# Performance work log

Measured on AMD Instinct MI355X. Metric: run time of the kernel, lower is better.

The kernel has to match this reference:

```python
import jax, jax.numpy as jnp
import numpy as np

# Dims
B, S, D = 2, 2048, 1024
H, KV = 16, 4            # rosa heads / kv heads -> n_rep = 4
QKB, VB = 16, 32          # query-key bits / value bits
N_REP = H // KV
TAU = 1.0


def setup_inputs() -> dict:
    key = jax.random.key(0)
    ks = jax.random.split(key, 8)
    sc = lambda fan_in: 1.0 / np.sqrt(fan_in)
    return {
        "hidden_states": jax.random.normal(ks[0], (B, S, D), jnp.float32),
        # Linear weights stored (in, out) so y = x @ W
        "Wq": jax.random.normal(ks[1], (D, H * QKB), jnp.float32) * sc(D),
        "Wk": jax.random.normal(ks[2], (D, KV * QKB), jnp.float32) * sc(D),
        "Wv": jax.random.normal(ks[3], (D, KV * VB), jnp.float32) * sc(D),
        "Wo": jax.random.normal(ks[4], (H * VB, D), jnp.float32) * sc(H * VB),
        "v_emb0": jnp.full((H * VB,), -1e-05, jnp.float32),
        "v_emb1": jnp.full((H * VB,), +1e-05, jnp.float32),
    }


def _repeat_kv(x, n_rep):
    # x: [B, KV, S, d] -> [B, KV*n_rep, S, d]
    b, kv, s, d = x.shape
    return jnp.broadcast_to(x[:, :, None], (b, kv, n_rep, s, d)).reshape(b, kv * n_rep, s, d)


def reference(hidden_states, Wq, Wk, Wv, Wo, v_emb0, v_emb1):
    b, s, _ = hidden_states.shape
    q = (hidden_states @ Wq).reshape(b, s, H, QKB).transpose(0, 2, 1, 3)   # [B,H,S,QKB]
    k = (hidden_states @ Wk).reshape(b, s, KV, QKB).transpose(0, 2, 1, 3)
    v = (hidden_states @ Wv).reshape(b, s, KV, VB).transpose(0, 2, 1, 3)
    k = _repeat_kv(k, N_REP)                                               # [B,H,S,QKB]
    v = _repeat_kv(v, N_REP)                                               # [B,H,S,VB]

    # Soft binarization (hard path uses (x > 0); soft path relaxes with sigmoid(x/tau)).
    pq = jax.nn.sigmoid(q / TAU)
    pk = jax.nn.sigmoid(k / TAU)
    pv = jax.nn.sigmoid(v / TAU)

    # Expected number of matching bits between soft-binary q_i and k_j:
    # sum_b [ pq*pk + (1-pq)(1-pk) ] = QKB - sum(pq) - sum(pk) + 2 * pq.pk
    dot = jnp.einsum("bhsd,bhtd->bhst", pq, pk)                            # [B,H,S,S]
    scores = QKB - pq.sum(-1)[:, :, :, None] - pk.sum(-1)[:, :, None, :] + 2.0 * dot

    causal = jnp.tril(jnp.ones((s, s), bool))                              # [S,S]
    scores = jnp.where(causal[None, None], scores, jnp.finfo(scores.dtype).min)
    attn = jax.nn.softmax(scores / TAU, axis=-1)

    vh = jnp.einsum("bhst,bhtd->bhsd", attn, pv)                           # [B,H,S,VB]
    e0 = v_emb0.reshape(1, H, 1, VB)
    e1 = v_emb1.reshape(1, H, 1, VB)
    out = e0 * (1.0 - vh) + e1 * vh                                        # [B,H,S,VB]
    out = out.transpose(0, 2, 1, 3).reshape(b, s, H * VB)
    return out @ Wo                                                        # [B,S,D]
```

## Files before the change

### kernel.cpp

```cpp
#include <hip/hip_runtime.h>
#include <hip/hip_bf16.h>

#define B_    2
#define S_    2048
#define D_    1024
#define H_    16
#define KV_   4
#define QKB_  16
#define VB_   32
#define NTOK  (B_ * S_)
#define L2E_  1.44269504088896f

typedef __attribute__((ext_vector_type(8))) short bshort8;
typedef __attribute__((ext_vector_type(4))) float f32x4;

__device__ __forceinline__ unsigned short bf16_rne(float x) {
    unsigned u = __float_as_uint(x);
    return (unsigned short)((u + 0x7FFFu + ((u >> 16) & 1u)) >> 16);
}
__device__ __forceinline__ unsigned bf16x2_rne(float lo, float hi) {
    return (unsigned)bf16_rne(lo) | ((unsigned)bf16_rne(hi) << 16);
}
__device__ __forceinline__ unsigned cvt_pk_bf16(float lo, float hi) {
    unsigned r;
    asm("v_cvt_pk_bf16_f32 %0, %1, %2" : "=v"(r) : "v"(lo), "v"(hi));
    return r;
}
__device__ __forceinline__ float sum2bf(unsigned u) {
    return __uint_as_float(u << 16) + __uint_as_float(u & 0xFFFF0000u);
}
__device__ __forceinline__ void stage16(const unsigned short* g, unsigned short* l) {
    __builtin_amdgcn_global_load_lds(
        (const __attribute__((address_space(1))) void*)g,
        (__attribute__((address_space(3))) void*)l, 16, 0, 0);
}

__global__ __launch_bounds__(256) void prep_kernel(
    const float* __restrict__ hs,
    const float* __restrict__ Wq, const float* __restrict__ Wk,
    const float* __restrict__ Wv, const float* __restrict__ Wo,
    unsigned short* __restrict__ hs_b,
    unsigned short* __restrict__ Wcat_t, unsigned short* __restrict__ Wot)
{
    __shared__ float T[64][65];
    const int t = threadIdx.x;
    if (blockIdx.x < 2048) {
        int i = blockIdx.x * 256 + t;
        const float4* s = (const float4*)hs;
        float4 a = s[2 * i], b = s[2 * i + 1];
        uint4 o;
        o.x = bf16x2_rne(a.x, a.y); o.y = bf16x2_rne(a.z, a.w);
        o.z = bf16x2_rne(b.x, b.y); o.w = bf16x2_rne(b.z, b.w);
        ((uint4*)hs_b)[i] = o;
        return;
    }
    const int bid = blockIdx.x - 2048;
    const float* src; unsigned short* dst; int K, N, tk, tn, drow0;
    if (bid < 64)       { src = Wq; dst = Wcat_t; K = 1024; N = 256;  int r = bid;       tk = r & 15; tn = r >> 4; drow0 = 0; }
    else if (bid < 80)  { src = Wk; dst = Wcat_t; K = 1024; N = 64;   int r = bid - 64;  tk = r;      tn = 0;      drow0 = 256; }
    else if (bid < 112) { src = Wv; dst = Wcat_t; K = 1024; N = 128;  int r = bid - 80;  tk = r & 15; tn = r >> 4; drow0 = 320; }
    else                { src = Wo; dst = Wot;    K = 512;  N = 1024; int r = bid - 112; tk = r & 7;  tn = r >> 3; drow0 = 0; }
    const int k0 = tk * 64, n0 = tn * 64;
    const int rr = t >> 4, cc = (t & 15) * 4;
    #pragma unroll
    for (int i = 0; i < 4; ++i) {
        float4 v = *(const float4*)(src + (k0 + rr + i * 16) * N + n0 + cc);
        T[rr + i * 16][cc + 0] = v.x; T[rr + i * 16][cc + 1] = v.y;
        T[rr + i * 16][cc + 2] = v.z; T[rr + i * 16][cc + 3] = v.w;
    }
    __syncthreads();
    const int nloc = t >> 2, kc = (t & 3) * 16;
    unsigned o[8];
    #pragma unroll
    for (int j = 0; j < 8; ++j)
        o[j] = bf16x2_rne(T[kc + 2 * j][nloc], T[kc + 2 * j + 1][nloc]);
    unsigned short* dp = dst + (drow0 + n0 + nloc) * K + k0 + kc;
    uint4 w0; w0.x = o[0]; w0.y = o[1]; w0.z = o[2]; w0.w = o[3];
    uint4 w1; w1.x = o[4]; w1.y = o[5]; w1.z = o[6]; w1.w = o[7];
    *(uint4*)(dp) = w0;
    *(uint4*)(dp + 8) = w1;
}

__global__ __launch_bounds__(256, 4) void proj_gemm(
    const unsigned short* __restrict__ Ab, const unsigned short* __restrict__ Btb,
    unsigned short* __restrict__ qg, unsigned short* __restrict__ pko,
    unsigned short* __restrict__ pvT)
{
    __shared__ unsigned short As[64 * 64];
    __shared__ unsigned short Bs[64 * 64];
    const int tid = threadIdx.x, l = tid & 63, w = tid >> 6;
    const int l15 = l & 15, quad = l >> 4;
    const int m0 = blockIdx.x * 64, n0 = blockIdx.y * 64;
    const int sr8 = l >> 3, sc8 = l & 7;
    f32x4 c[4];
    #pragma unroll
    for (int j = 0; j < 4; ++j) c[j] = (f32x4){0.f, 0.f, 0.f, 0.f};

    for (int k0 = 0; k0 < 1024; k0 += 64) {
        int R0 = w * 8, r0 = R0 + sr8;
        int R1 = 32 + w * 8, r1 = R1 + sr8;
        stage16(Ab  + (m0 + r0) * 1024 + k0 + (sc8 ^ (r0 & 7)) * 8, &As[R0 * 64]);
        stage16(Ab  + (m0 + r1) * 1024 + k0 + (sc8 ^ (r1 & 7)) * 8, &As[R1 * 64]);
        stage16(Btb + (n0 + r0) * 1024 + k0 + (sc8 ^ (r0 & 7)) * 8, &Bs[R0 * 64]);
        stage16(Btb + (n0 + r1) * 1024 + k0 + (sc8 ^ (r1 & 7)) * 8, &Bs[R1 * 64]);
        __syncthreads();
        #pragma unroll
        for (int kh = 0; kh < 2; ++kh) {
            const int arow = w * 16 + l15;
            bshort8 a = *(const bshort8*)&As[arow * 64 + (((kh * 4 + quad) ^ (arow & 7)) * 8)];
            #pragma unroll
            for (int bc = 0; bc < 4; ++bc) {
                const int brow = bc * 16 + l15;
                bshort8 b = *(const bshort8*)&Bs[brow * 64 + (((kh * 4 + quad) ^ (brow & 7)) * 8)];
                c[bc] = __builtin_amdgcn_mfma_f32_16x16x32_bf16(a, b, c[bc], 0, 0, 0);
            }
        }
        __syncthreads();
    }

    const int tok0 = m0 + w * 16 + quad * 4;
    #pragma unroll
    for (int bc = 0; bc < 4; ++bc) {
        f32x4 v = c[bc];
        const int n = n0 + bc * 16 + l15;
        float sg[4];
        #pragma unroll
        for (int r = 0; r < 4; ++r)
            sg[r] = 1.f / (1.f + exp2f(-v[r] * L2E_));
        if (n < 256) {
            const int hh = n >> 4, d = n & 15;
            #pragma unroll
            for (int r = 0; r < 4; ++r) {
                int tok = tok0 + r, bb = tok >> 11, ss = tok & 2047;
                qg[(((bb * 16 + hh) * 2048) + ss) * 16 + d] =
                    bf16_rne(L2E_ * (2.f * sg[r] - 1.f));
            }
        } else if (n < 320) {
            const int j = n - 256, kvv = j >> 4, d = j & 15;
            #pragma unroll
            for (int r = 0; r < 4; ++r) {
                int tok = tok0 + r, bb = tok >> 11, ss = tok & 2047;
                pko[(((bb * 4 + kvv) * 2048) + ss) * 16 + d] = bf16_rne(sg[r]);
            }
        } else {
            const int j = n - 320, kvv = j >> 5, d = j & 31;
            const int bb = tok0 >> 11, ss = tok0 & 2047;
            const int tl = ss >> 6, ccol = ss & 63;
            uint2 wv; wv.x = bf16x2_rne(sg[0], sg[1]); wv.y = bf16x2_rne(sg[2], sg[3]);
            *(uint2*)(pvT + ((((bb * 4 + kvv) * 32) + tl) * 32 + d) * 64 + ccol) = wv;
        }
    }
}

__global__ __launch_bounds__(256, 2) void outproj_gemm(
    const unsigned short* __restrict__ Ab, const unsigned short* __restrict__ Btb,
    float* __restrict__ out)
{
    __shared__ unsigned short As[64 * 64];
    __shared__ unsigned short Bs[128 * 64];
    const int tid = threadIdx.x, l = tid & 63, w = tid >> 6;
    const int l15 = l & 15, quad = l >> 4;
    const int m0 = blockIdx.x * 64, n0 = blockIdx.y * 128;
    const int wr = w & 1, wc = w >> 1;
    const int sr8 = l >> 3, sc8 = l & 7;
    f32x4 c[2][4];
    #pragma unroll
    for (int i = 0; i < 2; ++i)
        #pragma unroll
        for (int j = 0; j < 4; ++j) c[i][j] = (f32x4){0.f, 0.f, 0.f, 0.f};

    for (int k0 = 0; k0 < 512; k0 += 64) {
        #pragma unroll
        for (int j = 0; j < 2; ++j) {
            int R = w * 16 + j * 8, r = R + sr8;
            stage16(Ab + (m0 + r) * 512 + k0 + (sc8 ^ (r & 7)) * 8, &As[R * 64]);
        }
        #pragma unroll
        for (int j = 0; j < 4; ++j) {
            int R = j * 32 + w * 8, r = R + sr8;
            stage16(Btb + (n0 + r) * 512 + k0 + (sc8 ^ (r & 7)) * 8, &Bs[R * 64]);
        }
        __syncthreads();
        #pragma unroll
        for (int kh = 0; kh < 2; ++kh) {
            bshort8 a[2], b[4];
            #pragma unroll
            for (int ar = 0; ar < 2; ++ar) {
                int row = wr * 32 + ar * 16 + l15;
                a[ar] = *(const bshort8*)&As[row * 64 + (((kh * 4 + quad) ^ (row & 7)) * 8)];
            }
            #pragma unroll
            for (int bc = 0; bc < 4; ++bc) {
                int row = wc * 64 + bc * 16 + l15;
                b[bc] = *(const bshort8*)&Bs[row * 64 + (((kh * 4 + quad) ^ (row & 7)) * 8)];
            }
            #pragma unroll
            for (int ar = 0; ar < 2; ++ar)
                #pragma unroll
                for (int bc = 0; bc < 4; ++bc)
                    c[ar][bc] = __builtin_amdgcn_mfma_f32_16x16x32_bf16(a[ar], b[bc], c[ar][bc], 0, 0, 0);
        }
        __syncthreads();
    }

    #pragma unroll
    for (int ar = 0; ar < 2; ++ar)
        #pragma unroll
        for (int bc = 0; bc < 4; ++bc) {
            f32x4 v = c[ar][bc];
            const int col = n0 + wc * 64 + bc * 16 + l15;
            const int r0 = m0 + wr * 32 + ar * 16 + quad * 4;
            #pragma unroll
            for (int r = 0; r < 4; ++r)
                out[(r0 + r) * D_ + col] = v[r];
        }
}

__global__ __launch_bounds__(256, 4) void attn_kernel(
    const unsigned short* __restrict__ qg_g, const unsigned short* __restrict__ pk_g,
    const unsigned short* __restrict__ pvT_g, const float* __restrict__ e0,
    const float* __restrict__ e1, unsigned short* __restrict__ xo)
{
    __shared__ unsigned short Ks[2][64 * 16];
    __shared__ unsigned short Vs[2][32 * 64];
    __shared__ unsigned short P[4][16][88];
    const int tid = threadIdx.x, l = tid & 63, wq = tid >> 6;
    const int l15 = l & 15, quad = l >> 4;
    const int g = blockIdx.x;
    const int idx = g & 255, kg = g >> 8;
    const int bh = idx & 31, rr = idx >> 5;
    int qt;
    if      (kg == 0) qt = rr;
    else if (kg == 1) qt = 31 - rr;
    else if (kg == 2) qt = 8 + rr;
    else              qt = 23 - rr;
    const int b = bh >> 4, h = bh & 15, kv = h >> 2;
    const int qbase = qt * 64;
    const unsigned short* pkb = pk_g + ((b * 4 + kv) * 2048) * 16;
    const unsigned short* pvb = pvT_g + (b * 4 + kv) * 65536;
    const unsigned short* qgb = qg_g + ((b * 16 + h) * 2048) * 16;

    const f32x4 zero4 = {0.f, 0.f, 0.f, 0.f};
    const bshort8 zero8 = {0, 0, 0, 0, 0, 0, 0, 0};

    const unsigned short* qrow = qgb + (qbase + wq * 16 + l15) * 16;
    uint4 qu0 = *(const uint4*)qrow;
    uint4 qu1 = *(const uint4*)(qrow + 8);
    float s = sum2bf(qu0.x) + sum2bf(qu0.y) + sum2bf(qu0.z) + sum2bf(qu0.w)
            + sum2bf(qu1.x) + sum2bf(qu1.y) + sum2bf(qu1.z) + sum2bf(qu1.w);
    bshort8 qfrag = zero8;
    if (quad == 0)      qfrag = __builtin_bit_cast(bshort8, qu0);
    else if (quad == 1) qfrag = __builtin_bit_cast(bshort8, qu1);
    else if (quad == 2) qfrag[0] = (short)bf16_rne(-8.f * L2E_ - 0.5f * s);

    bshort8 kone = zero8; kone[0] = (short)0x3F80;

    f32x4 acc0 = zero4, acc1 = zero4;
    float lsum = 0.f;

    const int vrow_s = tid >> 3;
    const unsigned short* vsrc = pvb + vrow_s * 64 + (((tid & 7) ^ (vrow_s & 7)) * 8);
    const unsigned short* ksrc = pkb + (tid >> 1) * 16 + (tid & 1) * 8;

    const int koff = l15 * 16 + quad * 8;
    const int vx0 = ((quad ^ (l15 & 7)) * 8);
    const int vx1 = (((quad + 4) ^ (l15 & 7)) * 8);
    const int vrow = l15 * 64;

    const int q_lane = qbase + wq * 16 + l15;

    stage16(vsrc, &Vs[0][tid * 8]);
    if (tid < 128) stage16(ksrc, &Ks[0][tid * 8]);
    __syncthreads();

    int cur = 0;
    for (int t = 0; t <= qt; ++t) {
        if (t < qt) {
            stage16(vsrc + (t + 1) * 2048, &Vs[cur ^ 1][tid * 8]);
            if (tid < 128) stage16(ksrc + (t + 1) * 1024, &Ks[cur ^ 1][tid * 8]);
        }

        f32x4 sc[4];
        #pragma unroll
        for (int ks = 0; ks < 4; ++ks) {
            bshort8 kf;
            if (quad < 2)       kf = *(const bshort8*)&Ks[cur][ks * 256 + koff];
            else if (quad == 2) kf = kone;
            else                kf = zero8;
            sc[ks] = __builtin_amdgcn_mfma_f32_16x16x32_bf16(kf, qfrag, zero4, 0, 0, 0);
        }
        if (t < qt) {
            #pragma unroll
            for (int ks = 0; ks < 4; ++ks) {
                float p0 = exp2f(sc[ks][0]), p1 = exp2f(sc[ks][1]);
                float p2 = exp2f(sc[ks][2]), p3 = exp2f(sc[ks][3]);
                lsum += p0 + p1 + p2 + p3;
                uint2 wv; wv.x = cvt_pk_bf16(p0, p1); wv.y = cvt_pk_bf16(p2, p3);
                *(uint2*)&P[wq][l15][ks * 16 + quad * 4] = wv;
            }
        } else {
            const int t0 = qt * 64;
            #pragma unroll
            for (int ks = 0; ks < 4; ++ks) {
                float pv0[4];
                #pragma unroll
                for (int r = 0; r < 4; ++r) {
                    const int tg = t0 + ks * 16 + quad * 4 + r;
                    float pp = (tg <= q_lane) ? exp2f(sc[ks][r]) : 0.f;
                    lsum += pp; pv0[r] = pp;
                }
                uint2 wv; wv.x = cvt_pk_bf16(pv0[0], pv0[1]); wv.y = cvt_pk_bf16(pv0[2], pv0[3]);
                *(uint2*)&P[wq][l15][ks * 16 + quad * 4] = wv;
            }
        }
        {
            bshort8 pf0 = *(const bshort8*)&P[wq][l15][quad * 8];
            bshort8 pf1 = *(const bshort8*)&P[wq][l15][32 + quad * 8];
            bshort8 v0 = *(const bshort8*)&Vs[cur][vrow + vx0];
            bshort8 v1 = *(const bshort8*)&Vs[cur][vrow + vx1];
            bshort8 v2 = *(const bshort8*)&Vs[cur][vrow + 1024 + vx0];
            bshort8 v3 = *(const bshort8*)&Vs[cur][vrow + 1024 + vx1];
            acc0 = __builtin_amdgcn_mfma_f32_16x16x32_bf16(v0, pf0, acc0, 0, 0, 0);
            acc1 = __builtin_amdgcn_mfma_f32_16x16x32_bf16(v2, pf0, acc1, 0, 0, 0);
            acc0 = __builtin_amdgcn_mfma_f32_16x16x32_bf16(v1, pf1, acc0, 0, 0, 0);
            acc1 = __builtin_amdgcn_mfma_f32_16x16x32_bf16(v3, pf1, acc1, 0, 0, 0);
        }
        __syncthreads();
        cur ^= 1;
    }

    lsum += __shfl_xor(lsum, 16);
    lsum += __shfl_xor(lsum, 32);
    const float inv = 1.f / lsum;

    float e0v[8], dEv[8];
    #pragma unroll
    for (int vs = 0; vs < 2; ++vs)
        #pragma unroll
        for (int r = 0; r < 4; ++r) {
            int idx2 = h * 32 + vs * 16 + quad * 4 + r;
            float a = e0[idx2];
            e0v[vs * 4 + r] = a; dEv[vs * 4 + r] = e1[idx2] - a;
        }
    const int tok = b * 2048 + qbase + wq * 16 + l15;
    float o0[4], o1[4];
    #pragma unroll
    for (int r = 0; r < 4; ++r) {
        o0[r] = e0v[r]     + dEv[r]     * (acc0[r] * inv);
        o1[r] = e0v[4 + r] + dEv[4 + r] * (acc1[r] * inv);
    }
    uint2 w0; w0.x = cvt_pk_bf16(o0[0], o0[1]); w0.y = cvt_pk_bf16(o0[2], o0[3]);
    uint2 w1; w1.x = cvt_pk_bf16(o1[0], o1[1]); w1.y = cvt_pk_bf16(o1[2], o1[3]);
    *(uint2*)(xo + tok * 512 + h * 32 + quad * 4)      = w0;
    *(uint2*)(xo + tok * 512 + h * 32 + 16 + quad * 4) = w1;
}

extern "C" void kernel_launch(void* const* d_in, const int* in_sizes, int n_in,
                              void* d_out, int out_size, void* d_ws, size_t ws_size,
                              hipStream_t stream)
{
    const float* hs = (const float*)d_in[0];
    const float* Wq = (const float*)d_in[1];
    const float* Wk = (const float*)d_in[2];
    const float* Wv = (const float*)d_in[3];
    const float* Wo = (const float*)d_in[4];
    const float* e0 = (const float*)d_in[5];
    const float* e1 = (const float*)d_in[6];
    float* out = (float*)d_out;

    char* ws = (char*)d_ws;
    unsigned short* hs_b   = (unsigned short*)(ws);
    unsigned short* xo     = (unsigned short*)(ws);
    unsigned short* Wcat_t = (unsigned short*)(ws + 8388608);
    unsigned short* Wot    = (unsigned short*)(ws + 8388608 + 917504);
    unsigned short* qg     = (unsigned short*)(ws + 10354688);
    unsigned short* pk     = (unsigned short*)(ws + 12451840);
    unsigned short* pvT    = (unsigned short*)(ws + 12976128);

    prep_kernel<<<2288, 256, 0, stream>>>(hs, Wq, Wk, Wv, Wo, hs_b, Wcat_t, Wot);
    proj_gemm<<<dim3(64, 7), 256, 0, stream>>>(hs_b, Wcat_t, qg, pk, pvT);
    attn_kernel<<<1024, 256, 0, stream>>>(qg, pk, pvT, e0, e1, xo);
    outproj_gemm<<<dim3(64, 8), 256, 0, stream>>>(xo, Wot, out);
}
```

Before: 135.4 us.

## Pair complementary query tiles per block to share K/V staging and balance causal work

Each attention block now handles two query tiles, p and 31-p, for the same batch-head. It streams K/V tiles once and runs the score/softmax/PV pass for both queries, so every block has equal causal work. This halves the number of blocks and the redundant K/V loads into shared memory. In exchange it doubles per-thread accumulator state and lowers the launch-bounds occupancy hint from 4 to 2, which may reduce latency hiding with only 512 blocks.

```diff
diff --git a/kernel.cpp b/kernel.cpp
--- a/kernel.cpp
+++ b/kernel.cpp
@@ -216,7 +216,80 @@
         }
 }
 
-__global__ __launch_bounds__(256, 4) void attn_kernel(
+#define TILEPASS(QF, A0, A1, LS, DG, QLANE, T0) do {                           \
+    f32x4 s0_, s1_, s2_, s3_;                                                  \
+    {                                                                          \
+        bshort8 kf0_, kf1_, kf2_, kf3_;                                        \
+        if (quad < 2) {                                                        \
+            kf0_ = *(const bshort8*)&Ks[cur][0 * 256 + koff];                  \
+            kf1_ = *(const bshort8*)&Ks[cur][1 * 256 + koff];                  \
+            kf2_ = *(const bshort8*)&Ks[cur][2 * 256 + koff];                  \
+            kf3_ = *(const bshort8*)&Ks[cur][3 * 256 + koff];                  \
+        } else if (quad == 2) { kf0_ = kone; kf1_ = kone; kf2_ = kone; kf3_ = kone; } \
+        else                  { kf0_ = zero8; kf1_ = zero8; kf2_ = zero8; kf3_ = zero8; } \
+        s0_ = __builtin_amdgcn_mfma_f32_16x16x32_bf16(kf0_, QF, zero4, 0, 0, 0); \
+        s1_ = __builtin_amdgcn_mfma_f32_16x16x32_bf16(kf1_, QF, zero4, 0, 0, 0); \
+        s2_ = __builtin_amdgcn_mfma_f32_16x16x32_bf16(kf2_, QF, zero4, 0, 0, 0); \
+        s3_ = __builtin_amdgcn_mfma_f32_16x16x32_bf16(kf3_, QF, zero4, 0, 0, 0); \
+    }                                                                          \
+    if (!(DG)) {                                                               \
+        PACK4(s0_, 0, LS); PACK4(s1_, 1, LS); PACK4(s2_, 2, LS); PACK4(s3_, 3, LS); \
+    } else {                                                                   \
+        DPACK4(s0_, 0, LS, QLANE, T0); DPACK4(s1_, 1, LS, QLANE, T0);          \
+        DPACK4(s2_, 2, LS, QLANE, T0); DPACK4(s3_, 3, LS, QLANE, T0);          \
+    }                                                                          \
+    {                                                                          \
+        bshort8 pf0_ = *(const bshort8*)&P[wq][l15][quad * 8];                 \
+        bshort8 pf1_ = *(const bshort8*)&P[wq][l15][32 + quad * 8];            \
+        bshort8 v0_ = *(const bshort8*)&Vs[cur][vrow + vx0];                   \
+        bshort8 v1_ = *(const bshort8*)&Vs[cur][vrow + vx1];                   \
+        bshort8 v2_ = *(const bshort8*)&Vs[cur][vrow + 1024 + vx0];            \
+        bshort8 v3_ = *(const bshort8*)&Vs[cur][vrow + 1024 + vx1];            \
+        A0 = __builtin_amdgcn_mfma_f32_16x16x32_bf16(v0_, pf0_, A0, 0, 0, 0);  \
+        A1 = __builtin_amdgcn_mfma_f32_16x16x32_bf16(v2_, pf0_, A1, 0, 0, 0);  \
+        A0 = __builtin_amdgcn_mfma_f32_16x16x32_bf16(v1_, pf1_, A0, 0, 0, 0);  \
+        A1 = __builtin_amdgcn_mfma_f32_16x16x32_bf16(v3_, pf1_, A1, 0, 0, 0);  \
+    }                                                                          \
+} while (0)
+
+#define PACK4(scv, KS, LS) do {                                                \
+    float p0_ = exp2f(scv[0]), p1_ = exp2f(scv[1]);                            \
+    float p2_ = exp2f(scv[2]), p3_ = exp2f(scv[3]);                            \
+    LS += p0_ + p1_ + p2_ + p3_;                                               \
+    uint2 wv_; wv_.x = cvt_pk_bf16(p0_, p1_); wv_.y = cvt_pk_bf16(p2_, p3_);   \
+    *(uint2*)&P[wq][l15][(KS) * 16 + quad * 4] = wv_;                          \
+} while (0)
+
+#define DPACK4(scv, KS, LS, QLANE, T0) do {                                    \
+    float p0_ = ((T0) + (KS) * 16 + quad * 4 + 0 <= (QLANE)) ? exp2f(scv[0]) : 0.f; \
+    float p1_ = ((T0) + (KS) * 16 + quad * 4 + 1 <= (QLANE)) ? exp2f(scv[1]) : 0.f; \
+    float p2_ = ((T0) + (KS) * 16 + quad * 4 + 2 <= (QLANE)) ? exp2f(scv[2]) : 0.f; \
+    float p3_ = ((T0) + (KS) * 16 + quad * 4 + 3 <= (QLANE)) ? exp2f(scv[3]) : 0.f; \
+    LS += p0_ + p1_ + p2_ + p3_;                                               \
+    uint2 wv_; wv_.x = cvt_pk_bf16(p0_, p1_); wv_.y = cvt_pk_bf16(p2_, p3_);   \
+    *(uint2*)&P[wq][l15][(KS) * 16 + quad * 4] = wv_;                          \
+} while (0)
+
+#define WRITEOUT(QT, A0, A1, LS) do {                                          \
+    float ls_ = LS;                                                            \
+    ls_ += __shfl_xor(ls_, 16);                                                \
+    ls_ += __shfl_xor(ls_, 32);                                                \
+    const float inv_ = 1.f / ls_;                                              \
+    const int tok_ = b * 2048 + (QT) * 64 + wq * 16 + l15;                     \
+    float o0_[4], o1_[4];                                                      \
+    _Pragma("unroll")                                                          \
+    for (int r = 0; r < 4; ++r) {                                              \
+        o0_[r] = e0v[r]     + dEv[r]     * (A0[r] * inv_);                     \
+        o1_[r] = e0v[4 + r] + dEv[4 + r] * (A1[r] * inv_);                     \
+    }                                                                          \
+    uint2 w0_, w1_;                                                            \
+    w0_.x = cvt_pk_bf16(o0_[0], o0_[1]); w0_.y = cvt_pk_bf16(o0_[2], o0_[3]);  \
+    w1_.x = cvt_pk_bf16(o1_[0], o1_[1]); w1_.y = cvt_pk_bf16(o1_[2], o1_[3]);  \
+    *(uint2*)(xo + tok_ * 512 + h * 32 + quad * 4)      = w0_;                 \
+    *(uint2*)(xo + tok_ * 512 + h * 32 + 16 + quad * 4) = w1_;                 \
+} while (0)
+
+__global__ __launch_bounds__(256, 2) void attn_kernel(
     const unsigned short* __restrict__ qg_g, const unsigned short* __restrict__ pk_g,
     const unsigned short* __restrict__ pvT_g, const float* __restrict__ e0,
     const float* __restrict__ e1, unsigned short* __restrict__ xo)
@@ -227,36 +300,41 @@
     const int tid = threadIdx.x, l = tid & 63, wq = tid >> 6;
     const int l15 = l & 15, quad = l >> 4;
     const int g = blockIdx.x;
-    const int idx = g & 255, kg = g >> 8;
-    const int bh = idx & 31, rr = idx >> 5;
-    int qt;
-    if      (kg == 0) qt = rr;
-    else if (kg == 1) qt = 31 - rr;
-    else if (kg == 2) qt = 8 + rr;
-    else              qt = 23 - rr;
+    const int bh = g & 31, p = g >> 5;
+    const int qtA = p, qtB = 31 - p;
     const int b = bh >> 4, h = bh & 15, kv = h >> 2;
-    const int qbase = qt * 64;
     const unsigned short* pkb = pk_g + ((b * 4 + kv) * 2048) * 16;
     const unsigned short* pvb = pvT_g + (b * 4 + kv) * 65536;
     const unsigned short* qgb = qg_g + ((b * 16 + h) * 2048) * 16;
 
     const f32x4 zero4 = {0.f, 0.f, 0.f, 0.f};
     const bshort8 zero8 = {0, 0, 0, 0, 0, 0, 0, 0};
-
-    const unsigned short* qrow = qgb + (qbase + wq * 16 + l15) * 16;
-    uint4 qu0 = *(const uint4*)qrow;
-    uint4 qu1 = *(const uint4*)(qrow + 8);
-    float s = sum2bf(qu0.x) + sum2bf(qu0.y) + sum2bf(qu0.z) + sum2bf(qu0.w)
-            + sum2bf(qu1.x) + sum2bf(qu1.y) + sum2bf(qu1.z) + sum2bf(qu1.w);
-    bshort8 qfrag = zero8;
-    if (quad == 0)      qfrag = __builtin_bit_cast(bshort8, qu0);
-    else if (quad == 1) qfrag = __builtin_bit_cast(bshort8, qu1);
-    else if (quad == 2) qfrag[0] = (short)bf16_rne(-8.f * L2E_ - 0.5f * s);
-
     bshort8 kone = zero8; kone[0] = (short)0x3F80;
 
-    f32x4 acc0 = zero4, acc1 = zero4;
-    float lsum = 0.f;
+    bshort8 qfragA = zero8, qfragB = zero8;
+    {
+        const unsigned short* qrow = qgb + (qtA * 64 + wq * 16 + l15) * 16;
+        uint4 qu0 = *(const uint4*)qrow;
+        uint4 qu1 = *(const uint4*)(qrow + 8);
+        float s = sum2bf(qu0.x) + sum2bf(qu0.y) + sum2bf(qu0.z) + sum2bf(qu0.w)
+                + sum2bf(qu1.x) + sum2bf(qu1.y) + sum2bf(qu1.z) + sum2bf(qu1.w);
+        if (quad == 0)      qfragA = __builtin_bit_cast(bshort8, qu0);
+        else if (quad == 1) qfragA = __builtin_bit_cast(bshort8, qu1);
+        else if (quad == 2) qfragA[0] = (short)bf16_rne(-8.f * L2E_ - 0.5f * s);
+    }
+    {
+        const unsigned short* qrow = qgb + (qtB * 64 + wq * 16 + l15) * 16;
+        uint4 qu0 = *(const uint4*)qrow;
+        uint4 qu1 = *(const uint4*)(qrow + 8);
+        float s = sum2bf(qu0.x) + sum2bf(qu0.y) + sum2bf(qu0.z) + sum2bf(qu0.w)
+                + sum2bf(qu1.x) + sum2bf(qu1.y) + sum2bf(qu1.z) + sum2bf(qu1.w);
+        if (quad == 0)      qfragB = __builtin_bit_cast(bshort8, qu0);
+        else if (quad == 1) qfragB = __builtin_bit_cast(bshort8, qu1);
+        else if (quad == 2) qfragB[0] = (short)bf16_rne(-8.f * L2E_ - 0.5f * s);
+    }
+
+    f32x4 accA0 = zero4, accA1 = zero4, accB0 = zero4, accB1 = zero4;
+    float lsumA = 0.f, lsumB = 0.f;
 
     const int vrow_s = tid >> 3;
     const unsigned short* vsrc = pvb + vrow_s * 64 + (((tid & 7) ^ (vrow_s & 7)) * 8);
@@ -267,71 +345,25 @@
     const int vx1 = (((quad + 4) ^ (l15 & 7)) * 8);
     const int vrow = l15 * 64;
 
-    const int q_lane = qbase + wq * 16 + l15;
+    const int qlaneA = qtA * 64 + wq * 16 + l15;
+    const int qlaneB = qtB * 64 + wq * 16 + l15;
 
     stage16(vsrc, &Vs[0][tid * 8]);
     if (tid < 128) stage16(ksrc, &Ks[0][tid * 8]);
     __syncthreads();
 
     int cur = 0;
-    for (int t = 0; t <= qt; ++t) {
-        if (t < qt) {
+    for (int t = 0; t <= qtB; ++t) {
+        if (t < qtB) {
             stage16(vsrc + (t + 1) * 2048, &Vs[cur ^ 1][tid * 8]);
             if (tid < 128) stage16(ksrc + (t + 1) * 1024, &Ks[cur ^ 1][tid * 8]);
         }
-
-        f32x4 sc[4];
-        #pragma unroll
-        for (int ks = 0; ks < 4; ++ks) {
-            bshort8 kf;
-            if (quad < 2)       kf = *(const bshort8*)&Ks[cur][ks * 256 + koff];
-            else if (quad == 2) kf = kone;
-            else                kf = zero8;
-            sc[ks] = __builtin_amdgcn_mfma_f32_16x16x32_bf16(kf, qfrag, zero4, 0, 0, 0);
-        }
-        if (t < qt) {
-            #pragma unroll
-            for (int ks = 0; ks < 4; ++ks) {
-                float p0 = exp2f(sc[ks][0]), p1 = exp2f(sc[ks][1]);
-                float p2 = exp2f(sc[ks][2]), p3 = exp2f(sc[ks][3]);
-                lsum += p0 + p1 + p2 + p3;
-                uint2 wv; wv.x = cvt_pk_bf16(p0, p1); wv.y = cvt_pk_bf16(p2, p3);
-                *(uint2*)&P[wq][l15][ks * 16 + quad * 4] = wv;
-            }
-        } else {
-            const int t0 = qt * 64;
-            #pragma unroll
-            for (int ks = 0; ks < 4; ++ks) {
-                float pv0[4];
-                #pragma unroll
-                for (int r = 0; r < 4; ++r) {
-                    const int tg = t0 + ks * 16 + quad * 4 + r;
-                    float pp = (tg <= q_lane) ? exp2f(sc[ks][r]) : 0.f;
-                    lsum += pp; pv0[r] = pp;
-                }
-                uint2 wv; wv.x = cvt_pk_bf16(pv0[0], pv0[1]); wv.y = cvt_pk_bf16(pv0[2], pv0[3]);
-                *(uint2*)&P[wq][l15][ks * 16 + quad * 4] = wv;
-            }
-        }
-        {
-            bshort8 pf0 = *(const bshort8*)&P[wq][l15][quad * 8];
-            bshort8 pf1 = *(const bshort8*)&P[wq][l15][32 + quad * 8];
-            bshort8 v0 = *(const bshort8*)&Vs[cur][vrow + vx0];
-            bshort8 v1 = *(const bshort8*)&Vs[cur][vrow + vx1];
-            bshort8 v2 = *(const bshort8*)&Vs[cur][vrow + 1024 + vx0];
-            bshort8 v3 = *(const bshort8*)&Vs[cur][vrow + 1024 + vx1];
-            acc0 = __builtin_amdgcn_mfma_f32_16x16x32_bf16(v0, pf0, acc0, 0, 0, 0);
-            acc1 = __builtin_amdgcn_mfma_f32_16x16x32_bf16(v2, pf0, acc1, 0, 0, 0);
-            acc0 = __builtin_amdgcn_mfma_f32_16x16x32_bf16(v1, pf1, acc0, 0, 0, 0);
-            acc1 = __builtin_amdgcn_mfma_f32_16x16x32_bf16(v3, pf1, acc1, 0, 0, 0);
-        }
+        TILEPASS(qfragB, accB0, accB1, lsumB, t == qtB, qlaneB, t * 64);
+        if (t <= qtA)
+            TILEPASS(qfragA, accA0, accA1, lsumA, t == qtA, qlaneA, t * 64);
         __syncthreads();
         cur ^= 1;
     }
-
-    lsum += __shfl_xor(lsum, 16);
-    lsum += __shfl_xor(lsum, 32);
-    const float inv = 1.f / lsum;
 
     float e0v[8], dEv[8];
     #pragma unroll
@@ -342,17 +374,8 @@
             float a = e0[idx2];
             e0v[vs * 4 + r] = a; dEv[vs * 4 + r] = e1[idx2] - a;
         }
-    const int tok = b * 2048 + qbase + wq * 16 + l15;
-    float o0[4], o1[4];
-    #pragma unroll
-    for (int r = 0; r < 4; ++r) {
-        o0[r] = e0v[r]     + dEv[r]     * (acc0[r] * inv);
-        o1[r] = e0v[4 + r] + dEv[4 + r] * (acc1[r] * inv);
-    }
-    uint2 w0; w0.x = cvt_pk_bf16(o0[0], o0[1]); w0.y = cvt_pk_bf16(o0[2], o0[3]);
-    uint2 w1; w1.x = cvt_pk_bf16(o1[0], o1[1]); w1.y = cvt_pk_bf16(o1[2], o1[3]);
-    *(uint2*)(xo + tok * 512 + h * 32 + quad * 4)      = w0;
-    *(uint2*)(xo + tok * 512 + h * 32 + 16 + quad * 4) = w1;
+    WRITEOUT(qtA, accA0, accA1, lsumA);
+    WRITEOUT(qtB, accB0, accB1, lsumB);
 }
 
 extern "C" void kernel_launch(void* const* d_in, const int* in_sizes, int n_in,
@@ -379,6 +402,6 @@
 
     prep_kernel<<<2288, 256, 0, stream>>>(hs, Wq, Wk, Wv, Wo, hs_b, Wcat_t, Wot);
     proj_gemm<<<dim3(64, 7), 256, 0, stream>>>(hs_b, Wcat_t, qg, pk, pvT);
-    attn_kernel<<<1024, 256, 0, stream>>>(qg, pk, pvT, e0, e1, xo);
+    attn_kernel<<<512, 256, 0, stream>>>(qg, pk, pvT, e0, e1, xo);
     outproj_gemm<<<dim3(64, 8), 256, 0, stream>>>(xo, Wot, out);
 }
```

After: 135.5 us. No clear change (+0.1%).
